# Optimization experiments

Hardware: AMD Instinct MI355X
Metric: run time of the kernel (lower is better)

## Reference

```python
import jax, jax.numpy as jnp
import numpy as np

N_NODES = 20000
N_EDGES = 160000
N_GRAPHS = 64
VOCAB = 2 ** 16
EMBED_DIM = 32
IN_GNN = EMBED_DIM + 4  # 36
H1, H2 = 2048, 1024
N_CLASSES = 2  # task 'a'


def setup_inputs() -> dict:
    key = jax.random.key(0)
    ks = jax.random.split(key, 16)
    inp = {
        "node_type_ids": jax.random.randint(ks[0], (N_NODES,), 0, VOCAB, dtype=jnp.int32),
        "other_feats": jax.random.normal(ks[1], (N_NODES, 4), dtype=jnp.float32),
        "edge_index": jax.random.randint(ks[2], (2, N_EDGES), 0, N_NODES, dtype=jnp.int32),
        "batch": jnp.sort(jax.random.randint(ks[3], (N_NODES,), 0, N_GRAPHS, dtype=jnp.int32)),
        # parameters
        "emb": jax.random.normal(ks[4], (VOCAB, EMBED_DIM), dtype=jnp.float32),
        "W1": jax.random.normal(ks[5], (IN_GNN, H1), dtype=jnp.float32) * 0.05,
        "b1": jnp.zeros((H1,), jnp.float32),
        "W2": jax.random.normal(ks[6], (H1, H2), dtype=jnp.float32) * 0.02,
        "b2": jnp.zeros((H2,), jnp.float32),
        "hW1": jax.random.normal(ks[7], (H2, 1024), dtype=jnp.float32) * 0.02,
        "hb1": jnp.zeros((1024,), jnp.float32),
        "hW2": jax.random.normal(ks[8], (1024, 512), dtype=jnp.float32) * 0.02,
        "hb2": jnp.zeros((512,), jnp.float32),
        "oW": jax.random.normal(ks[9], (512, N_CLASSES), dtype=jnp.float32) * 0.02,
        "ob": jnp.zeros((N_CLASSES,), jnp.float32),
    }
    return inp


def _gcn_conv(x, W, b, src, dst, dinv):
    # PyG GCNConv (add_self_loops already applied in src/dst, dinv precomputed):
    # out_i = sum_{j->i} dinv[j]*dinv[i] * (x_j @ W) + b
    xw = x @ W  # [N, out]
    norm = dinv[src] * dinv[dst]  # [E']
    msg = xw[src] * norm[:, None]  # [E', out] -- dominant HBM traffic
    out = jax.ops.segment_sum(msg, dst, num_segments=x.shape[0])
    return out + b


def _forward(node_type_ids, other_feats, edge_index, batch,
             emb, W1, b1, W2, b2, hW1, hb1, hW2, hb2, oW, ob):
    n = other_feats.shape[0]
    # add self-loops (gcn_norm default)
    loop = jnp.arange(n, dtype=edge_index.dtype)
    src = jnp.concatenate([edge_index[0], loop])
    dst = jnp.concatenate([edge_index[1], loop])
    deg = jax.ops.segment_sum(jnp.ones(src.shape[0], other_feats.dtype), dst, num_segments=n)
    dinv = jnp.where(deg > 0, jax.lax.rsqrt(deg), 0.0)

    x = jnp.concatenate([emb[node_type_ids], other_feats], axis=-1)  # [N, 36]
    x = jax.nn.relu(_gcn_conv(x, W1, b1, src, dst, dinv))  # dropout is eval no-op
    x = jax.nn.relu(_gcn_conv(x, W2, b2, src, dst, dinv))

    # global mean pool over graphs
    counts = jax.ops.segment_sum(jnp.ones(n, x.dtype), batch, num_segments=N_GRAPHS)
    pooled = jax.ops.segment_sum(x, batch, num_segments=N_GRAPHS)
    pooled = pooled / jnp.maximum(counts, 1.0)[:, None]  # [G, 1024]

    h = jax.nn.relu(pooled @ hW1 + hb1)
    h = jax.nn.relu(h @ hW2 + hb2)
    return h @ oW + ob  # [G, 2]


def reference(node_type_ids, other_feats, edge_index, batch,
              emb, W1, b1, W2, b2, hW1, hb1, hW2, hb2, oW, ob):
    return _forward(node_type_ids, other_feats, edge_index, batch,
                    emb, W1, b1, W2, b2, hW1, hb1, hW2, hb2, oW, ob)
```

## Files before the change

### kernel.cpp

```cpp
#include <hip/hip_runtime.h>
#include <hip/hip_bf16.h>

#define N_NODES  20000
#define N_EDGES  160000
#define N_TOT_E  180000
#define N_GRAPHS 64
#define EMBED_DIM 32
#define IN_GNN   36
#define K1PAD    64
#define H1       2048
#define H2       1024
#define CHUNK0   10112

typedef unsigned short u16;
typedef short bf16x8 __attribute__((ext_vector_type(8)));
typedef float f32x4  __attribute__((ext_vector_type(4)));

__device__ inline u16 f32_to_bf16(float f) {
    union { float f; unsigned u; } v; v.f = f;
    unsigned lsb = (v.u >> 16) & 1u;
    return (u16)((v.u + 0x7fffu + lsb) >> 16);
}
__device__ inline float bf16_to_f32(u16 h) {
    union { unsigned u; float f; } v; v.u = ((unsigned)h) << 16;
    return v.f;
}


__global__ void fill_i32(int* p, int v, int n) {
    int i = blockIdx.x * 256 + threadIdx.x;
    if (i < n) p[i] = v;
}

__global__ void deg_accum(const int* __restrict__ ei, int* indeg) {
    int e = blockIdx.x * 256 + threadIdx.x;
    if (e < N_EDGES) atomicAdd(&indeg[ei[N_EDGES + e]], 1);
}

__global__ void deg_to_dinv(const int* __restrict__ indeg, float* __restrict__ d) {
    int i = blockIdx.x * 256 + threadIdx.x;
    if (i < N_NODES) d[i] = rsqrtf((float)indeg[i]);
}

__global__ void build_xfeat(const int* __restrict__ ids, const float* __restrict__ other,
                            const float* __restrict__ emb, float* __restrict__ xf) {
    int idx = blockIdx.x * 256 + threadIdx.x;
    if (idx >= N_NODES * IN_GNN) return;
    int i = idx / IN_GNN;
    int d = idx - i * IN_GNN;
    float v = (d < EMBED_DIM) ? emb[(size_t)ids[i] * EMBED_DIM + d]
                              : other[i * 4 + (d - EMBED_DIM)];
    xf[idx] = v;
}

__global__ __launch_bounds__(1024) void scan_offsets(const int* __restrict__ indeg,
                                                     int* __restrict__ off,
                                                     int* __restrict__ cursor) {
    __shared__ int buf[1024];
    __shared__ int base_s;
    int tid = threadIdx.x;
    if (tid == 0) base_s = 0;
    __syncthreads();
    for (int start = 0; start < N_NODES; start += 1024) {
        int i = start + tid;
        int v = (i < N_NODES) ? indeg[i] : 0;
        buf[tid] = v;
        __syncthreads();
        for (int s = 1; s < 1024; s <<= 1) {
            int t = (tid >= s) ? buf[tid - s] : 0;
            __syncthreads();
            buf[tid] += t;
            __syncthreads();
        }
        int incl = buf[tid];
        int excl = incl - v;
        int base = base_s;
        if (i < N_NODES) {
            int o = base + excl;
            off[i] = o;
            cursor[i] = o;
        }
        __syncthreads();
        if (tid == 1023) base_s = base + incl;
        __syncthreads();
    }
    if (tid == 0) off[N_NODES] = N_TOT_E;
}

__global__ void csr_fill(const int* __restrict__ ei, const float* __restrict__ dinv,
                         int* __restrict__ cursor,
                         int* __restrict__ csr_src, float* __restrict__ csr_nrm) {
    int e = blockIdx.x * 256 + threadIdx.x;
    if (e >= N_TOT_E) return;
    int s, t;
    if (e < N_EDGES) { s = ei[e]; t = ei[N_EDGES + e]; }
    else             { s = t = e - N_EDGES; }
    int pos = atomicAdd(&cursor[t], 1);
    csr_src[pos] = s;
    csr_nrm[pos] = dinv[s] * dinv[t];
}

__global__ void agg_csr_36(const int* __restrict__ off, const int* __restrict__ csr_src,
                           const float* __restrict__ csr_nrm,
                           const float* __restrict__ xf,
                           u16* __restrict__ aggh, u16* __restrict__ aggl) {
    int idx = blockIdx.x * 256 + threadIdx.x;
    if (idx >= N_NODES * K1PAD) return;
    int node = idx >> 6;
    int d = idx & 63;
    u16 hi = 0, lo = 0;
    if (d < IN_GNN) {
        int p0 = off[node], p1 = off[node + 1];
        float acc = 0.0f;
        for (int p = p0; p < p1; p++)
            acc += xf[csr_src[p] * IN_GNN + d] * csr_nrm[p];
        hi = f32_to_bf16(acc);
        lo = f32_to_bf16(acc - bf16_to_f32(hi));
    }
    aggh[idx] = hi;
    aggl[idx] = lo;
}

__global__ void conv_w1(const float* __restrict__ W,
                        u16* __restrict__ Bh, u16* __restrict__ Bl) {
    int idx = blockIdx.x * 256 + threadIdx.x;
    if (idx >= H1 * K1PAD) return;
    int n = idx >> 6;
    int k = idx & 63;
    u16 hi = 0, lo = 0;
    if (k < IN_GNN) {
        float v = W[(size_t)k * H1 + n];
        hi = f32_to_bf16(v);
        lo = f32_to_bf16(v - bf16_to_f32(hi));
    }
    Bh[idx] = hi;
    Bl[idx] = lo;
}

__global__ __launch_bounds__(256) void conv_w2(const float* __restrict__ W,
                                               u16* __restrict__ Bh,
                                               u16* __restrict__ Bl) {
    __shared__ float t[32][33];
    int bk = blockIdx.x * 32;
    int bn = blockIdx.y * 32;
    int tx = threadIdx.x & 31, ty = threadIdx.x >> 5;
#pragma unroll
    for (int i = 0; i < 32; i += 8)
        t[ty + i][tx] = W[(size_t)(bk + ty + i) * H2 + bn + tx];
    __syncthreads();
#pragma unroll
    for (int i = 0; i < 32; i += 8) {
        float v = t[tx][ty + i];
        u16 hi = f32_to_bf16(v);
        u16 lo = f32_to_bf16(v - bf16_to_f32(hi));
        size_t o = (size_t)(bn + ty + i) * H1 + bk + tx;
        Bh[o] = hi;
        Bl[o] = lo;
    }
}

__global__ __launch_bounds__(256) void gemm1_mfma(const u16* __restrict__ Ah,
                                                  const u16* __restrict__ Al,
                                                  const u16* __restrict__ Bh,
                                                  const u16* __restrict__ Bl,
                                                  const float* __restrict__ bias,
                                                  u16* __restrict__ Xh,
                                                  u16* __restrict__ Xl,
                                                  int rowbase, int nrows) {
    __shared__ u16 lds[4][128 * K1PAD];
    const int tid  = threadIdx.x;
    const int wid  = tid >> 6;
    const int lane = tid & 63;
    const int wr   = wid >> 1, wc = wid & 1;
    const int row0 = blockIdx.y * 128;
    const int col0 = blockIdx.x * 128;

    const u16* gbase;
    int rbase; bool isA;
    if      (wid == 0) { gbase = Ah; rbase = row0; isA = true; }
    else if (wid == 1) { gbase = Al; rbase = row0; isA = true; }
    else if (wid == 2) { gbase = Bh; rbase = col0; isA = false; }
    else               { gbase = Bl; rbase = col0; isA = false; }
    u16* myl = lds[wid];
    const int r_l  = lane >> 3;
    const int ks_l = (lane & 7) * 8;
#pragma unroll
    for (int i = 0; i < 16; i++) {
        int r = rbase + i * 8 + r_l;
        if (isA) { int g = rowbase + ((r > nrows - 1) ? (nrows - 1) : r);
                   r = g; }
        const u16* g = gbase + (size_t)r * K1PAD + ks_l;
        __builtin_amdgcn_global_load_lds(
            (const __attribute__((address_space(1))) void*)g,
            (__attribute__((address_space(3))) void*)(myl + i * 512),
            16, 0, 0);
    }
    __syncthreads();

    f32x4 acc[4][4] = {};
#pragma unroll
    for (int ks = 0; ks < 2; ks++) {
        bf16x8 afh[4], afl[4];
#pragma unroll
        for (int mi = 0; mi < 4; mi++) {
            int r   = wr * 64 + mi * 16 + (lane & 15);
            int off = r * K1PAD + ks * 32 + (lane >> 4) * 8;
            afh[mi] = *(const bf16x8*)&lds[0][off];
            afl[mi] = *(const bf16x8*)&lds[1][off];
        }
#pragma unroll
        for (int ni = 0; ni < 4; ni++) {
            int c   = wc * 64 + ni * 16 + (lane & 15);
            int off = c * K1PAD + ks * 32 + (lane >> 4) * 8;
            bf16x8 bfh = *(const bf16x8*)&lds[2][off];
            bf16x8 bfl = *(const bf16x8*)&lds[3][off];
#pragma unroll
            for (int mi = 0; mi < 4; mi++) {
                acc[mi][ni] = __builtin_amdgcn_mfma_f32_16x16x32_bf16(afh[mi], bfh, acc[mi][ni], 0, 0, 0);
                acc[mi][ni] = __builtin_amdgcn_mfma_f32_16x16x32_bf16(afh[mi], bfl, acc[mi][ni], 0, 0, 0);
                acc[mi][ni] = __builtin_amdgcn_mfma_f32_16x16x32_bf16(afl[mi], bfh, acc[mi][ni], 0, 0, 0);
            }
        }
    }

#pragma unroll
    for (int ni = 0; ni < 4; ni++) {
        int col = col0 + wc * 64 + ni * 16 + (lane & 15);
        float bb = bias[col];
#pragma unroll
        for (int mi = 0; mi < 4; mi++) {
#pragma unroll
            for (int j = 0; j < 4; j++) {
                int lr = row0 + wr * 64 + mi * 16 + (lane >> 4) * 4 + j;
                if (lr < nrows) {
                    float v = fmaxf(acc[mi][ni][j] + bb, 0.0f);
                    u16 hi = f32_to_bf16(v);
                    Xh[(size_t)lr * H1 + col] = hi;
                    Xl[(size_t)lr * H1 + col] = f32_to_bf16(v - bf16_to_f32(hi));
                }
            }
        }
    }
}

__global__ __launch_bounds__(256) void gemm2_mfma(const u16* __restrict__ Ah,
                                                  const u16* __restrict__ Al,
                                                  const u16* __restrict__ Bh,
                                                  const u16* __restrict__ Bl,
                                                  float* __restrict__ C,
                                                  int rowbase, int nrows) {
    __shared__ u16 lds[4][128 * 32];
    const int tid  = threadIdx.x;
    const int wid  = tid >> 6;
    const int lane = tid & 63;
    const int wr   = wid >> 1, wc = wid & 1;

    int NB = (int)(gridDim.x * gridDim.y);
    int b  = (int)(blockIdx.y * gridDim.x + blockIdx.x);
    int lin = b;
    if ((NB & 7) == 0) {
        int xcd = b & 7, j = b >> 3;
        lin = xcd * (NB >> 3) + j;
    }
    const int col0 = (lin & 7) * 128;
    const int row0 = (lin >> 3) * 128;

    const u16* gbase;
    int rbase;
    if      (wid == 0) { gbase = Ah; rbase = row0; }
    else if (wid == 1) { gbase = Al; rbase = row0; }
    else if (wid == 2) { gbase = Bh; rbase = col0; }
    else               { gbase = Bl; rbase = col0; }
    u16* myl = lds[wid];
    const int r_l  = lane >> 2;
    const int ks_l = (lane & 3) * 8;

    int rows[8];
#pragma unroll
    for (int i = 0; i < 8; i++) {
        int r = rbase + i * 16 + r_l;
        if (wid < 2 && r > nrows - 1) r = nrows - 1;
        rows[i] = r;
    }

    f32x4 acc[4][4] = {};

    for (int kt = 0; kt < H1 / 32; ++kt) {
        int k0 = kt * 32;
        __syncthreads();
#pragma unroll
        for (int i = 0; i < 8; i++) {
            const u16* g = gbase + (size_t)rows[i] * H1 + k0 + ks_l;
            __builtin_amdgcn_global_load_lds(
                (const __attribute__((address_space(1))) void*)g,
                (__attribute__((address_space(3))) void*)(myl + i * 512),
                16, 0, 0);
        }
        __syncthreads();

        bf16x8 afh[4], afl[4];
#pragma unroll
        for (int mi = 0; mi < 4; mi++) {
            int r   = wr * 64 + mi * 16 + (lane & 15);
            int off = r * 32 + (lane >> 4) * 8;
            afh[mi] = *(const bf16x8*)&lds[0][off];
            afl[mi] = *(const bf16x8*)&lds[1][off];
        }
#pragma unroll
        for (int ni = 0; ni < 4; ni++) {
            int c   = wc * 64 + ni * 16 + (lane & 15);
            int off = c * 32 + (lane >> 4) * 8;
            bf16x8 bfh = *(const bf16x8*)&lds[2][off];
            bf16x8 bfl = *(const bf16x8*)&lds[3][off];
#pragma unroll
            for (int mi = 0; mi < 4; mi++) {
                acc[mi][ni] = __builtin_amdgcn_mfma_f32_16x16x32_bf16(afh[mi], bfh, acc[mi][ni], 0, 0, 0);
                acc[mi][ni] = __builtin_amdgcn_mfma_f32_16x16x32_bf16(afh[mi], bfl, acc[mi][ni], 0, 0, 0);
                acc[mi][ni] = __builtin_amdgcn_mfma_f32_16x16x32_bf16(afl[mi], bfh, acc[mi][ni], 0, 0, 0);
            }
        }
    }

#pragma unroll
    for (int mi = 0; mi < 4; mi++) {
#pragma unroll
        for (int ni = 0; ni < 4; ni++) {
            int col = col0 + wc * 64 + ni * 16 + (lane & 15);
#pragma unroll
            for (int j = 0; j < 4; j++) {
                int lr = row0 + wr * 64 + mi * 16 + (lane >> 4) * 4 + j;
                if (lr < nrows) C[(size_t)(rowbase + lr) * H2 + col] = acc[mi][ni][j];
            }
        }
    }
}

__global__ __launch_bounds__(256) void agg_csr_1024(const int* __restrict__ off,
                                                    const int* __restrict__ csr_src,
                                                    const float* __restrict__ csr_nrm,
                                                    const float* __restrict__ xw,
                                                    const float* __restrict__ b,
                                                    float* __restrict__ x2) {
    int node = blockIdx.x;
    int p0 = off[node], p1 = off[node + 1];
    int d = threadIdx.x;
    float4 a0 = make_float4(0.f, 0.f, 0.f, 0.f);
    float4 a1 = make_float4(0.f, 0.f, 0.f, 0.f);
    int p = p0;
    for (; p + 1 < p1; p += 2) {
        int   s0 = csr_src[p],     s1 = csr_src[p + 1];
        float n0 = csr_nrm[p],     n1 = csr_nrm[p + 1];
        float4 v0 = ((const float4*)&xw[(size_t)s0 * H2])[d];
        float4 v1 = ((const float4*)&xw[(size_t)s1 * H2])[d];
        a0.x += v0.x * n0; a0.y += v0.y * n0; a0.z += v0.z * n0; a0.w += v0.w * n0;
        a1.x += v1.x * n1; a1.y += v1.y * n1; a1.z += v1.z * n1; a1.w += v1.w * n1;
    }
    if (p < p1) {
        int   s0 = csr_src[p];
        float n0 = csr_nrm[p];
        float4 v0 = ((const float4*)&xw[(size_t)s0 * H2])[d];
        a0.x += v0.x * n0; a0.y += v0.y * n0; a0.z += v0.z * n0; a0.w += v0.w * n0;
    }
    float4 bb = ((const float4*)b)[d];
    float4 o;
    o.x = fmaxf(a0.x + a1.x + bb.x, 0.f);
    o.y = fmaxf(a0.y + a1.y + bb.y, 0.f);
    o.z = fmaxf(a0.z + a1.z + bb.z, 0.f);
    o.w = fmaxf(a0.w + a1.w + bb.w, 0.f);
    ((float4*)&x2[(size_t)node * H2])[d] = o;
}

__global__ void cnt_accum(const int* __restrict__ batch, float* cnt) {
    int i = blockIdx.x * 256 + threadIdx.x;
    if (i < N_NODES) atomicAdd(&cnt[batch[i]], 1.0f);
}

__global__ void pool_accum(const int* __restrict__ batch, const float* __restrict__ x2,
                           float* __restrict__ pooled) {
    int d  = blockIdx.x * 256 + threadIdx.x;
    int i0 = blockIdx.y * 64;
    float acc = 0.0f;
    int gprev = -1;
    for (int i = 0; i < 64; i++) {
        int node = i0 + i;
        if (node >= N_NODES) break;
        int g = batch[node];
        if (g != gprev) {
            if (gprev >= 0) atomicAdd(&pooled[gprev * H2 + d], acc);
            acc = 0.0f; gprev = g;
        }
        acc += x2[(size_t)node * H2 + d];
    }
    if (gprev >= 0) atomicAdd(&pooled[gprev * H2 + d], acc);
}

__global__ void pool_norm(float* pooled, const float* cnt) {
    int idx = blockIdx.x * 256 + threadIdx.x;
    if (idx < N_GRAPHS * H2) {
        int g = idx >> 10;
        pooled[idx] /= fmaxf(cnt[g], 1.0f);
    }
}

__global__ __launch_bounds__(256) void head_gemm(const float* __restrict__ In,
                                                 const float* __restrict__ W,
                                                 float* __restrict__ Out, int K, int N) {
    __shared__ __align__(16) float As[16][256];
    int n  = blockIdx.x * 256 + threadIdx.x;
    int m0 = blockIdx.y * 16;
    int k0 = blockIdx.z * 256;
    for (int t = threadIdx.x; t < 16 * 256; t += 256) {
        int r = t >> 8, k = t & 255;
        As[r][k] = In[(size_t)(m0 + r) * K + k0 + k];
    }
    __syncthreads();
    float acc[16] = {};
    for (int k = 0; k < 256; k += 4) {
        float w0 = W[(size_t)(k0 + k + 0) * N + n];
        float w1 = W[(size_t)(k0 + k + 1) * N + n];
        float w2 = W[(size_t)(k0 + k + 2) * N + n];
        float w3 = W[(size_t)(k0 + k + 3) * N + n];
#pragma unroll
        for (int r = 0; r < 16; r++) {
            float4 a = *(const float4*)&As[r][k];
            acc[r] += a.x * w0 + a.y * w1 + a.z * w2 + a.w * w3;
        }
    }
    for (int r = 0; r < 16; r++)
        atomicAdd(&Out[(size_t)(m0 + r) * N + n], acc[r]);
}

__global__ void bias_relu_MN(float* __restrict__ x, const float* __restrict__ b,
                             int N, int total) {
    int idx = blockIdx.x * 256 + threadIdx.x;
    if (idx < total) {
        int d = idx & (N - 1);
        x[idx] = fmaxf(x[idx] + b[d], 0.0f);
    }
}

__global__ void head3(const float* __restrict__ h2, const float* __restrict__ oW,
                      const float* __restrict__ ob, float* __restrict__ out) {
    int tid = threadIdx.x;
    if (tid >= 128) return;
    int m = tid >> 1, c = tid & 1;
    float acc = 0.0f;
    for (int k = 0; k < 512; k++) acc += h2[m * 512 + k] * oW[k * 2 + c];
    out[tid] = acc + ob[c];
}

extern "C" void kernel_launch(void* const* d_in, const int* in_sizes, int n_in,
                              void* d_out, int out_size, void* d_ws, size_t ws_size,
                              hipStream_t stream) {
    const int*   ids   = (const int*)d_in[0];
    const float* other = (const float*)d_in[1];
    const int*   ei    = (const int*)d_in[2];
    const int*   batch = (const int*)d_in[3];
    const float* emb   = (const float*)d_in[4];
    const float* W1    = (const float*)d_in[5];
    const float* b1    = (const float*)d_in[6];
    const float* W2    = (const float*)d_in[7];
    const float* b2    = (const float*)d_in[8];
    const float* hW1   = (const float*)d_in[9];
    const float* hb1   = (const float*)d_in[10];
    const float* hW2   = (const float*)d_in[11];
    const float* hb2   = (const float*)d_in[12];
    const float* oW    = (const float*)d_in[13];
    const float* ob    = (const float*)d_in[14];
    float* out = (float*)d_out;

    char* ws = (char*)d_ws;
    size_t off_b = 0;
    auto alloc = [&](size_t bytes) {
        size_t p = (off_b + 255) & ~(size_t)255;
        off_b = p + bytes;
        return p;
    };
    size_t o_dinv = alloc((size_t)N_NODES * 4);
    size_t o_indeg= alloc((size_t)(N_NODES + 1) * 4);
    size_t o_off  = alloc((size_t)(N_NODES + 1) * 4);
    size_t o_cur  = alloc((size_t)N_NODES * 4);
    size_t o_csrc = alloc((size_t)N_TOT_E * 4);
    size_t o_cnrm = alloc((size_t)N_TOT_E * 4);
    size_t o_xf   = alloc((size_t)N_NODES * IN_GNN * 4);
    size_t o_aggh = alloc((size_t)N_NODES * K1PAD * 2);
    size_t o_aggl = alloc((size_t)N_NODES * K1PAD * 2);
    size_t o_w1h  = alloc((size_t)H1 * K1PAD * 2);
    size_t o_w1l  = alloc((size_t)H1 * K1PAD * 2);
    size_t o_x1h  = alloc((size_t)CHUNK0 * H1 * 2);
    size_t o_x1l  = alloc((size_t)CHUNK0 * H1 * 2);
    size_t o_w2h  = alloc((size_t)H2 * H1 * 2);
    size_t o_w2l  = alloc((size_t)H2 * H1 * 2);
    size_t o_xw2  = alloc((size_t)N_NODES * H2 * 4);
    size_t o_pool = alloc((size_t)N_GRAPHS * H2 * 4);
    size_t o_cnt  = alloc((size_t)N_GRAPHS * 4);
    size_t o_h1   = alloc((size_t)N_GRAPHS * 1024 * 4);
    size_t o_h2   = alloc((size_t)N_GRAPHS * 512 * 4);

    float* dinv = (float*)(ws + o_dinv);
    int*   indeg= (int*)(ws + o_indeg);
    int*   offs = (int*)(ws + o_off);
    int*   cur  = (int*)(ws + o_cur);
    int*   csrc = (int*)(ws + o_csrc);
    float* cnrm = (float*)(ws + o_cnrm);
    float* xf   = (float*)(ws + o_xf);
    u16*   aggh = (u16*)(ws + o_aggh);
    u16*   aggl = (u16*)(ws + o_aggl);
    u16*   w1h  = (u16*)(ws + o_w1h);
    u16*   w1l  = (u16*)(ws + o_w1l);
    u16*   x1h  = (u16*)(ws + o_x1h);
    u16*   x1l  = (u16*)(ws + o_x1l);
    u16*   w2h  = (u16*)(ws + o_w2h);
    u16*   w2l  = (u16*)(ws + o_w2l);
    float* xw2  = (float*)(ws + o_xw2);
    float* x2   = (float*)(ws + o_x1h);
    float* pooled = (float*)(ws + o_pool);
    float* cnt  = (float*)(ws + o_cnt);
    float* h1   = (float*)(ws + o_h1);
    float* h2   = (float*)(ws + o_h2);

    fill_i32<<<(N_NODES + 255) / 256, 256, 0, stream>>>(indeg, 1, N_NODES);
    deg_accum<<<(N_EDGES + 255) / 256, 256, 0, stream>>>(ei, indeg);
    deg_to_dinv<<<(N_NODES + 255) / 256, 256, 0, stream>>>(indeg, dinv);

    scan_offsets<<<1, 1024, 0, stream>>>(indeg, offs, cur);
    csr_fill<<<(N_TOT_E + 255) / 256, 256, 0, stream>>>(ei, dinv, cur, csrc, cnrm);

    build_xfeat<<<(N_NODES * IN_GNN + 255) / 256, 256, 0, stream>>>(ids, other, emb, xf);
    agg_csr_36<<<(N_NODES * K1PAD + 255) / 256, 256, 0, stream>>>(offs, csrc, cnrm, xf, aggh, aggl);

    conv_w1<<<(H1 * K1PAD + 255) / 256, 256, 0, stream>>>(W1, w1h, w1l);
    conv_w2<<<dim3(H1 / 32, H2 / 32), 256, 0, stream>>>(W2, w2h, w2l);

    {
        const int c0 = CHUNK0, c1 = N_NODES - CHUNK0;
        gemm1_mfma<<<dim3(H1 / 128, c0 / 128), 256, 0, stream>>>(aggh, aggl, w1h, w1l, b1, x1h, x1l, 0, c0);
        gemm2_mfma<<<dim3(H2 / 128, c0 / 128), 256, 0, stream>>>(x1h, x1l, w2h, w2l, xw2, 0, c0);
        gemm1_mfma<<<dim3(H1 / 128, (c1 + 127) / 128), 256, 0, stream>>>(aggh, aggl, w1h, w1l, b1, x1h, x1l, c0, c1);
        gemm2_mfma<<<dim3(H2 / 128, (c1 + 127) / 128), 256, 0, stream>>>(x1h, x1l, w2h, w2l, xw2, c0, c1);
    }

    agg_csr_1024<<<N_NODES, 256, 0, stream>>>(offs, csrc, cnrm, xw2, b2, x2);

    hipMemsetAsync(pooled, 0, (size_t)N_GRAPHS * H2 * 4, stream);
    hipMemsetAsync(cnt, 0, (size_t)N_GRAPHS * 4, stream);
    cnt_accum<<<(N_NODES + 255) / 256, 256, 0, stream>>>(batch, cnt);
    pool_accum<<<dim3(H2 / 256, (N_NODES + 63) / 64), 256, 0, stream>>>(batch, x2, pooled);
    pool_norm<<<(N_GRAPHS * H2 + 255) / 256, 256, 0, stream>>>(pooled, cnt);

    hipMemsetAsync(h1, 0, (size_t)N_GRAPHS * 1024 * 4, stream);
    head_gemm<<<dim3(1024 / 256, 4, 1024 / 256), 256, 0, stream>>>(pooled, hW1, h1, 1024, 1024);
    bias_relu_MN<<<(N_GRAPHS * 1024 + 255) / 256, 256, 0, stream>>>(h1, hb1, 1024, N_GRAPHS * 1024);

    hipMemsetAsync(h2, 0, (size_t)N_GRAPHS * 512 * 4, stream);
    head_gemm<<<dim3(512 / 256, 4, 1024 / 256), 256, 0, stream>>>(h1, hW2, h2, 1024, 512);
    bias_relu_MN<<<(N_GRAPHS * 512 + 255) / 256, 256, 0, stream>>>(h2, hb2, 512, N_GRAPHS * 512);

    head3<<<1, 128, 0, stream>>>(h2, oW, ob, out);
}
```

Measured before the change: 935.8 us.

## Narrow gemm2 tiles, warp-shuffle offset scan, and fuse head GEMMs with bias/relu

The gemm2 MFMA kernel moves from 128x128 to 128x64 output tiles, which doubles the block count and halves the per-wave accumulator footprint. The aim is better occupancy and less tail imbalance, at the price of re-reading the A operand for twice as many column tiles. The single-block offset scan now uses wave-level shuffle scans plus a small cross-wave scan, replacing a barrier-heavy Hillis-Steele loop in LDS. The head MLP layers loop over K inside one kernel and apply bias and ReLU directly, which removes the memsets, atomics and separate bias kernels but gives fewer blocks per launch.

New measurement: 1.249 ms. 33.5% more time.

```diff
diff --git a/kernel.cpp b/kernel.cpp
--- a/kernel.cpp
+++ b/kernel.cpp
@@ -56,33 +56,37 @@
 __global__ __launch_bounds__(1024) void scan_offsets(const int* __restrict__ indeg,
                                                      int* __restrict__ off,
                                                      int* __restrict__ cursor) {
-    __shared__ int buf[1024];
-    __shared__ int base_s;
+    __shared__ int wsum[16];
     int tid = threadIdx.x;
-    if (tid == 0) base_s = 0;
-    __syncthreads();
+    int lane = tid & 63, wid = tid >> 6;
+    int base = 0;
     for (int start = 0; start < N_NODES; start += 1024) {
         int i = start + tid;
         int v = (i < N_NODES) ? indeg[i] : 0;
-        buf[tid] = v;
-        __syncthreads();
-        for (int s = 1; s < 1024; s <<= 1) {
-            int t = (tid >= s) ? buf[tid - s] : 0;
-            __syncthreads();
-            buf[tid] += t;
-            __syncthreads();
-        }
-        int incl = buf[tid];
-        int excl = incl - v;
-        int base = base_s;
-        if (i < N_NODES) {
-            int o = base + excl;
-            off[i] = o;
-            cursor[i] = o;
-        }
-        __syncthreads();
-        if (tid == 1023) base_s = base + incl;
-        __syncthreads();
+        int x = v;
+#pragma unroll
+        for (int d = 1; d < 64; d <<= 1) {
+            int y = __shfl_up(x, d);
+            if (lane >= d) x += y;
+        }
+        if (lane == 63) wsum[wid] = x;
+        __syncthreads();
+        if (wid == 0 && lane < 16) {
+            int w = wsum[lane];
+#pragma unroll
+            for (int d = 1; d < 16; d <<= 1) {
+                int y = __shfl_up(w, d, 16);
+                if ((lane & 15) >= d) w += y;
+            }
+            wsum[lane] = w;
+        }
+        __syncthreads();
+        int incl = x + (wid > 0 ? wsum[wid - 1] : 0);
+        int excl = base + incl - v;
+        if (i < N_NODES) { off[i] = excl; cursor[i] = excl; }
+        int total = wsum[15];
+        __syncthreads();
+        base += total;
     }
     if (tid == 0) off[N_NODES] = N_TOT_E;
 }
@@ -249,7 +253,8 @@
                                                   const u16* __restrict__ Bl,
                                                   float* __restrict__ C,
                                                   int rowbase, int nrows) {
-    __shared__ u16 lds[4][128 * 32];
+    __shared__ u16 ldsAh[128 * 32], ldsAl[128 * 32];
+    __shared__ u16 ldsBh[64 * 32],  ldsBl[64 * 32];
     const int tid  = threadIdx.x;
     const int wid  = tid >> 6;
     const int lane = tid & 63;
@@ -257,21 +262,18 @@
 
     int NB = (int)(gridDim.x * gridDim.y);
     int b  = (int)(blockIdx.y * gridDim.x + blockIdx.x);
-    int lin = b;
-    if ((NB & 7) == 0) {
-        int xcd = b & 7, j = b >> 3;
-        lin = xcd * (NB >> 3) + j;
-    }
-    const int col0 = (lin & 7) * 128;
-    const int row0 = (lin >> 3) * 128;
+    int q  = NB >> 3;
+    int lin = (b & 7) * q + (b >> 3);
+    const int col0 = (lin & 15) * 64;
+    const int row0 = (lin >> 4) * 128;
 
     const u16* gbase;
+    u16* myl;
     int rbase;
-    if      (wid == 0) { gbase = Ah; rbase = row0; }
-    else if (wid == 1) { gbase = Al; rbase = row0; }
-    else if (wid == 2) { gbase = Bh; rbase = col0; }
-    else               { gbase = Bl; rbase = col0; }
-    u16* myl = lds[wid];
+    if      (wid == 0) { gbase = Ah; myl = ldsAh; rbase = row0; }
+    else if (wid == 1) { gbase = Al; myl = ldsAl; rbase = row0; }
+    else if (wid == 2) { gbase = Bh; myl = ldsBh; rbase = col0; }
+    else               { gbase = Bl; myl = ldsBl; rbase = col0; }
     const int r_l  = lane >> 2;
     const int ks_l = (lane & 3) * 8;
 
@@ -282,14 +284,14 @@
         if (wid < 2 && r > nrows - 1) r = nrows - 1;
         rows[i] = r;
     }
-
-    f32x4 acc[4][4] = {};
+    const int nstage = (wid < 2) ? 8 : 4;
+
+    f32x4 acc[4][2] = {};
 
     for (int kt = 0; kt < H1 / 32; ++kt) {
         int k0 = kt * 32;
         __syncthreads();
-#pragma unroll
-        for (int i = 0; i < 8; i++) {
+        for (int i = 0; i < nstage; i++) {
             const u16* g = gbase + (size_t)rows[i] * H1 + k0 + ks_l;
             __builtin_amdgcn_global_load_lds(
                 (const __attribute__((address_space(1))) void*)g,
@@ -303,15 +305,15 @@
         for (int mi = 0; mi < 4; mi++) {
             int r   = wr * 64 + mi * 16 + (lane & 15);
             int off = r * 32 + (lane >> 4) * 8;
-            afh[mi] = *(const bf16x8*)&lds[0][off];
-            afl[mi] = *(const bf16x8*)&lds[1][off];
-        }
-#pragma unroll
-        for (int ni = 0; ni < 4; ni++) {
-            int c   = wc * 64 + ni * 16 + (lane & 15);
+            afh[mi] = *(const bf16x8*)&ldsAh[off];
+            afl[mi] = *(const bf16x8*)&ldsAl[off];
+        }
+#pragma unroll
+        for (int ni = 0; ni < 2; ni++) {
+            int c   = wc * 32 + ni * 16 + (lane & 15);
             int off = c * 32 + (lane >> 4) * 8;
-            bf16x8 bfh = *(const bf16x8*)&lds[2][off];
-            bf16x8 bfl = *(const bf16x8*)&lds[3][off];
+            bf16x8 bfh = *(const bf16x8*)&ldsBh[off];
+            bf16x8 bfl = *(const bf16x8*)&ldsBl[off];
 #pragma unroll
             for (int mi = 0; mi < 4; mi++) {
                 acc[mi][ni] = __builtin_amdgcn_mfma_f32_16x16x32_bf16(afh[mi], bfh, acc[mi][ni], 0, 0, 0);
@@ -324,8 +326,8 @@
 #pragma unroll
     for (int mi = 0; mi < 4; mi++) {
 #pragma unroll
-        for (int ni = 0; ni < 4; ni++) {
-            int col = col0 + wc * 64 + ni * 16 + (lane & 15);
+        for (int ni = 0; ni < 2; ni++) {
+            int col = col0 + wc * 32 + ni * 16 + (lane & 15);
 #pragma unroll
             for (int j = 0; j < 4; j++) {
                 int lr = row0 + wr * 64 + mi * 16 + (lane >> 4) * 4 + j;
@@ -402,40 +404,39 @@
     }
 }
 
-__global__ __launch_bounds__(256) void head_gemm(const float* __restrict__ In,
-                                                 const float* __restrict__ W,
-                                                 float* __restrict__ Out, int K, int N) {
+__global__ __launch_bounds__(256) void head_fused(const float* __restrict__ In,
+                                                  const float* __restrict__ W,
+                                                  const float* __restrict__ bias,
+                                                  float* __restrict__ Out,
+                                                  int K, int N, int relu) {
     __shared__ __align__(16) float As[16][256];
     int n  = blockIdx.x * 256 + threadIdx.x;
     int m0 = blockIdx.y * 16;
-    int k0 = blockIdx.z * 256;
-    for (int t = threadIdx.x; t < 16 * 256; t += 256) {
-        int r = t >> 8, k = t & 255;
-        As[r][k] = In[(size_t)(m0 + r) * K + k0 + k];
-    }
-    __syncthreads();
     float acc[16] = {};
-    for (int k = 0; k < 256; k += 4) {
-        float w0 = W[(size_t)(k0 + k + 0) * N + n];
-        float w1 = W[(size_t)(k0 + k + 1) * N + n];
-        float w2 = W[(size_t)(k0 + k + 2) * N + n];
-        float w3 = W[(size_t)(k0 + k + 3) * N + n];
-#pragma unroll
-        for (int r = 0; r < 16; r++) {
-            float4 a = *(const float4*)&As[r][k];
-            acc[r] += a.x * w0 + a.y * w1 + a.z * w2 + a.w * w3;
-        }
-    }
-    for (int r = 0; r < 16; r++)
-        atomicAdd(&Out[(size_t)(m0 + r) * N + n], acc[r]);
-}
-
-__global__ void bias_relu_MN(float* __restrict__ x, const float* __restrict__ b,
-                             int N, int total) {
-    int idx = blockIdx.x * 256 + threadIdx.x;
-    if (idx < total) {
-        int d = idx & (N - 1);
-        x[idx] = fmaxf(x[idx] + b[d], 0.0f);
+    for (int k0 = 0; k0 < K; k0 += 256) {
+        __syncthreads();
+        for (int t = threadIdx.x; t < 16 * 256; t += 256) {
+            int r = t >> 8, k = t & 255;
+            As[r][k] = In[(size_t)(m0 + r) * K + k0 + k];
+        }
+        __syncthreads();
+        for (int k = 0; k < 256; k += 4) {
+            float w0 = W[(size_t)(k0 + k + 0) * N + n];
+            float w1 = W[(size_t)(k0 + k + 1) * N + n];
+            float w2 = W[(size_t)(k0 + k + 2) * N + n];
+            float w3 = W[(size_t)(k0 + k + 3) * N + n];
+#pragma unroll
+            for (int r = 0; r < 16; r++) {
+                float4 a = *(const float4*)&As[r][k];
+                acc[r] += a.x * w0 + a.y * w1 + a.z * w2 + a.w * w3;
+            }
+        }
+    }
+    float bb = bias[n];
+    for (int r = 0; r < 16; r++) {
+        float v = acc[r] + bb;
+        if (relu) v = fmaxf(v, 0.0f);
+        Out[(size_t)(m0 + r) * N + n] = v;
     }
 }
 
@@ -535,9 +536,9 @@
     {
         const int c0 = CHUNK0, c1 = N_NODES - CHUNK0;
         gemm1_mfma<<<dim3(H1 / 128, c0 / 128), 256, 0, stream>>>(aggh, aggl, w1h, w1l, b1, x1h, x1l, 0, c0);
-        gemm2_mfma<<<dim3(H2 / 128, c0 / 128), 256, 0, stream>>>(x1h, x1l, w2h, w2l, xw2, 0, c0);
+        gemm2_mfma<<<dim3(16, c0 / 128), 256, 0, stream>>>(x1h, x1l, w2h, w2l, xw2, 0, c0);
         gemm1_mfma<<<dim3(H1 / 128, (c1 + 127) / 128), 256, 0, stream>>>(aggh, aggl, w1h, w1l, b1, x1h, x1l, c0, c1);
-        gemm2_mfma<<<dim3(H2 / 128, (c1 + 127) / 128), 256, 0, stream>>>(x1h, x1l, w2h, w2l, xw2, c0, c1);
+        gemm2_mfma<<<dim3(16, (c1 + 127) / 128), 256, 0, stream>>>(x1h, x1l, w2h, w2l, xw2, c0, c1);
     }
 
     agg_csr_1024<<<N_NODES, 256, 0, stream>>>(offs, csrc, cnrm, xw2, b2, x2);
@@ -548,13 +549,7 @@
     pool_accum<<<dim3(H2 / 256, (N_NODES + 63) / 64), 256, 0, stream>>>(batch, x2, pooled);
     pool_norm<<<(N_GRAPHS * H2 + 255) / 256, 256, 0, stream>>>(pooled, cnt);
 
-    hipMemsetAsync(h1, 0, (size_t)N_GRAPHS * 1024 * 4, stream);
-    head_gemm<<<dim3(1024 / 256, 4, 1024 / 256), 256, 0, stream>>>(pooled, hW1, h1, 1024, 1024);
-    bias_relu_MN<<<(N_GRAPHS * 1024 + 255) / 256, 256, 0, stream>>>(h1, hb1, 1024, N_GRAPHS * 1024);
-
-    hipMemsetAsync(h2, 0, (size_t)N_GRAPHS * 512 * 4, stream);
-    head_gemm<<<dim3(512 / 256, 4, 1024 / 256), 256, 0, stream>>>(h1, hW2, h2, 1024, 512);
-    bias_relu_MN<<<(N_GRAPHS * 512 + 255) / 256, 256, 0, stream>>>(h2, hb2, 512, N_GRAPHS * 512);
-
+    head_fused<<<dim3(1024 / 256, N_GRAPHS / 16), 256, 0, stream>>>(pooled, hW1, hb1, h1, 1024, 1024, 1);
+    head_fused<<<dim3(512 / 256, N_GRAPHS / 16), 256, 0, stream>>>(h1, hW2, hb2, h2, 1024, 512, 1);
     head3<<<1, 128, 0, stream>>>(h2, oW, ob, out);
 }
```
